# Performance work log

Measured on AMD Instinct MI355X. Metric: run time of the kernel, lower is better.

The kernel has to match this reference:

```python
import jax, jax.numpy as jnp
import numpy as np

B, T_IN, T_OUT = 32, 256, 512
N_MEL, E = 80, 512
A_RNN, D_RNN, PRENET, A_DIM = 1024, 1024, 256, 128
N_FILT, KSIZE = 32, 31


def setup_inputs() -> dict:
    key = jax.random.key(0)
    ks = jax.random.split(key, 20)
    def w(k, shape):
        fan_in = shape[-1] if len(shape) == 2 else shape[1] * shape[2]
        return jax.random.normal(k, shape, jnp.float32) / np.sqrt(fan_in)
    return dict(
        memory=jax.random.normal(ks[0], (B, T_IN, E), jnp.float32),
        decoder_inputs=jax.random.normal(ks[1], (B, N_MEL, T_OUT), jnp.float32),
        memory_lengths=jax.random.randint(ks[2], (B,), T_IN // 2, T_IN + 1).astype(jnp.int32),
        prenet_w1=w(ks[3], (PRENET, N_MEL)),
        prenet_w2=w(ks[4], (PRENET, PRENET)),
        att_rnn_wih=w(ks[5], (4 * A_RNN, PRENET + E)),
        att_rnn_whh=w(ks[6], (4 * A_RNN, A_RNN)),
        att_rnn_b=jnp.zeros((4 * A_RNN,), jnp.float32),
        wq=w(ks[7], (A_DIM, A_RNN)),
        wm=w(ks[8], (A_DIM, E)),
        v=w(ks[9], (1, A_DIM)),
        loc_conv=w(ks[10], (N_FILT, 2, KSIZE)),
        loc_dense=w(ks[11], (A_DIM, N_FILT)),
        dec_rnn_wih=w(ks[12], (4 * D_RNN, A_RNN + E)),
        dec_rnn_whh=w(ks[13], (4 * D_RNN, D_RNN)),
        dec_rnn_b=jnp.zeros((4 * D_RNN,), jnp.float32),
        proj_w=w(ks[14], (N_MEL, D_RNN + E)),
        proj_b=jnp.zeros((N_MEL,), jnp.float32),
        gate_w=w(ks[15], (1, D_RNN + E)),
        gate_b=jnp.zeros((1,), jnp.float32),
    )


def _lstm_cell(x, h, c, wih, whh, b):
    g = x @ wih.T + h @ whh.T + b
    i, f, gg, o = jnp.split(g, 4, axis=-1)
    c2 = jax.nn.sigmoid(f) * c + jax.nn.sigmoid(i) * jnp.tanh(gg)
    h2 = jax.nn.sigmoid(o) * jnp.tanh(c2)
    return h2, c2


def reference(memory, decoder_inputs, memory_lengths, prenet_w1, prenet_w2,
              att_rnn_wih, att_rnn_whh, att_rnn_b, wq, wm, v, loc_conv, loc_dense,
              dec_rnn_wih, dec_rnn_whh, dec_rnn_b, proj_w, proj_b, gate_w, gate_b):
    Bc, Tin, Ec = memory.shape
    # True where padded (masked out of attention)
    pad_mask = jnp.arange(Tin)[None, :] >= memory_lengths[:, None]
    processed_memory = memory @ wm.T  # (B, T_in, A_DIM)

    # parse decoder inputs: (B, n_mel, T_out) -> (T_out, B, n_mel); prepend go frame
    dec_seq = jnp.transpose(decoder_inputs, (2, 0, 1))
    go = jnp.zeros((1, Bc, N_MEL), dec_seq.dtype)
    dec_seq = jnp.concatenate([go, dec_seq], axis=0)[:-1]  # teacher-forced inputs
    # prenet (eval; stochastic dropout removed for determinism)
    x = jax.nn.relu(dec_seq @ prenet_w1.T)
    x = jax.nn.relu(x @ prenet_w2.T)  # (T_out, B, PRENET)

    NEG = jnp.asarray(-1e9, memory.dtype)
    pad = KSIZE // 2

    def step(carry, xt):
        ah, ac, dh, dc, aw, awc, ctx = carry
        # attention RNN
        ah, ac = _lstm_cell(jnp.concatenate([xt, ctx], -1), ah, ac,
                            att_rnn_wih, att_rnn_whh, att_rnn_b)
        # location-sensitive attention
        cat = jnp.stack([aw, awc], axis=1)  # (B, 2, T_in)
        loc = jax.lax.conv_general_dilated(cat, loc_conv, (1,), [(pad, pad)],
                                           dimension_numbers=('NCH', 'OIH', 'NCH'))
        loc = jnp.transpose(loc, (0, 2, 1)) @ loc_dense.T  # (B, T_in, A_DIM)
        pq = ah @ wq.T  # (B, A_DIM)
        e = jnp.tanh(pq[:, None, :] + loc + processed_memory) @ v[0]  # (B, T_in)
        e = jnp.where(pad_mask, NEG, e)
        wgt = jax.nn.softmax(e, axis=1)
        ctx = jnp.einsum('bt,bte->be', wgt, memory)
        awc = awc + wgt
        # decoder RNN
        dh, dc = _lstm_cell(jnp.concatenate([ah, ctx], -1), dh, dc,
                            dec_rnn_wih, dec_rnn_whh, dec_rnn_b)
        pi = jnp.concatenate([dh, ctx], -1)
        mel = pi @ proj_w.T + proj_b
        gate = (pi @ gate_w.T + gate_b)[:, 0]
        return (ah, ac, dh, dc, wgt, awc, ctx), (mel, gate, wgt)

    z = lambda *s: jnp.zeros(s, memory.dtype)
    carry0 = (z(Bc, A_RNN), z(Bc, A_RNN), z(Bc, D_RNN), z(Bc, D_RNN),
              z(Bc, Tin), z(Bc, Tin), z(Bc, Ec))
    _, (mels, gates, aligns) = jax.lax.scan(step, carry0, x)
    mel_out = jnp.transpose(mels, (1, 2, 0))      # (B, n_mel, T_out)
    gate_out = gates.T                             # (B, T_out)
    align_out = jnp.transpose(aligns, (1, 0, 2))   # (B, T_out, T_in)
    return mel_out, gate_out, align_out
```

## Files before the change

### kernel.cpp

```cpp
#include <hip/hip_runtime.h>
#include <hip/hip_bf16.h>
#include <math.h>

typedef __attribute__((ext_vector_type(8))) short bf16x8;
typedef __attribute__((ext_vector_type(4))) float f32x4;

#define B_X2    0u
#define B_PM    8388608u
#define B_WSA   12582912u
#define B_WSD   27262976u
#define B_AHB0  48234496u
#define B_AHB1  48300032u
#define B_DHB0  48365568u
#define B_DHB1  48431104u
#define B_CTXB  48496640u
#define B_AC    48529408u
#define B_DC    48660480u
#define B_AWC   48791552u
#define B_ZERO_START 48234496u
#define B_ZERO_BYTES 589824u
#define B_AHF   48824320u
#define B_DHF0  48955392u
#define B_CTXF0 49086464u
#define B_CTXF1 49152000u
#define B_DHF1  49217536u
#define B_LPM   49348608u
#define B_WQT   53542912u

#define OUT_MEL   0u
#define OUT_GATE  1310720u
#define OUT_ALIGN 1327104u

#define PSM_BYTES 6144

#define QSM_BYTES 23040

__device__ __forceinline__ float sigf(float x) { return 1.f / (1.f + expf(-x)); }
__device__ __forceinline__ float ftanh(float x) {
    float t = exp2f(x * 2.885390081777927f);
    return 1.f - 2.f * __builtin_amdgcn_rcpf(t + 1.f);
}

#define HOLD(s, b0, b1) (((s) & 1) ? (b0) : (b1))

__global__ __launch_bounds__(256) void prenet_kernel(
    const float* __restrict__ dec_in,
    const float* __restrict__ w1,
    const float* __restrict__ w2,
    __hip_bfloat16* __restrict__ x2)
{
    int b  = blockIdx.x & 31;
    int t0 = (blockIdx.x >> 5) * 16;
    __shared__ float xin[16][80];
    __shared__ float h1[16][257];

    for (int i = threadIdx.x; i < 16 * 80; i += 256) {
        int tt = i / 80, m = i - tt * 80;
        int t = t0 + tt;
        xin[tt][m] = (t == 0) ? 0.f
                   : dec_in[(size_t)b * 80 * 512 + (size_t)m * 512 + (t - 1)];
    }
    __syncthreads();
    for (int i = threadIdx.x; i < 16 * 256; i += 256) {
        int tt = i >> 8, p = i & 255;
        const float* wr = w1 + p * 80;
        float s = 0.f;
        for (int m = 0; m < 80; ++m) s += xin[tt][m] * wr[m];
        h1[tt][p] = fmaxf(s, 0.f);
    }
    __syncthreads();
    for (int i = threadIdx.x; i < 16 * 256; i += 256) {
        int tt = i >> 8, q = i & 255;
        const float* wr = w2 + q * 256;
        float s = 0.f;
        for (int p = 0; p < 256; ++p) s += h1[tt][p] * wr[p];
        int t = t0 + tt;
        x2[(size_t)t * (32 * 256) + b * 256 + q] = __float2bfloat16(fmaxf(s, 0.f));
    }
}

__global__ __launch_bounds__(128) void pm_kernel(
    const float* __restrict__ memory,
    const float* __restrict__ wm,
    float* __restrict__ pm)
{
    int b = blockIdx.y, tt0 = blockIdx.x * 16;
    __shared__ float ms[16][513];
    for (int i = threadIdx.x; i < 16 * 512; i += 128) {
        int tt = i >> 9, e = i & 511;
        ms[tt][e] = memory[(size_t)b * 131072 + (size_t)(tt0 + tt) * 512 + e];
    }
    __syncthreads();
    int d = threadIdx.x;
    float acc[16];
#pragma unroll
    for (int i = 0; i < 16; ++i) acc[i] = 0.f;
    const float* wr = wm + d * 512;
    for (int e = 0; e < 512; ++e) {
        float w = wr[e];
#pragma unroll
        for (int ttl = 0; ttl < 16; ++ttl) acc[ttl] += w * ms[ttl][e];
    }
    for (int ttl = 0; ttl < 16; ++ttl)
        pm[(size_t)b * 32768 + (size_t)(tt0 + ttl) * 128 + d] = acc[ttl];
}

__global__ __launch_bounds__(256) void swizzle_kernel(
    const float* __restrict__ wih, int Kih,
    const float* __restrict__ whh, int Khh,
    __hip_bfloat16* __restrict__ out, int K)
{
    int idx = blockIdx.x * 256 + threadIdx.x;
    int lane = idx & 63;
    int tk = idx >> 6;
    int KB = K >> 5;
    int nt = tk / KB, kb = tk - nt * KB;
    int c = lane & 15;
    int n = (c >> 2) * 1024 + nt * 4 + (c & 3);
    int k = kb * 32 + ((lane >> 4) << 3);
    const float* src; int kk;
    if (k < Kih) { src = wih + (size_t)n * Kih; kk = k; }
    else         { src = whh + (size_t)n * Khh; kk = k - Kih; }
    __hip_bfloat16* op = out + (size_t)idx * 8;
#pragma unroll
    for (int j = 0; j < 8; ++j) op[j] = __float2bfloat16(src[kk + j]);
}

__global__ __launch_bounds__(256) void wqt_kernel(
    const float* __restrict__ wq,
    float* __restrict__ wqT)
{
    int idx = blockIdx.x * 256 + threadIdx.x;
    int k = idx >> 7, d = idx & 127;
    wqT[idx] = wq[(size_t)d * 1024 + k];
}

template<int K, int S0, int S1, int S0STR, int S1STR, int S2STR>
__device__ __forceinline__ void lstm_tile(
    char* smem, int nt,
    const __hip_bfloat16* __restrict__ seg0,
    const __hip_bfloat16* __restrict__ seg1,
    const __hip_bfloat16* __restrict__ seg2,
    const __hip_bfloat16* __restrict__ wsw,
    const float* __restrict__ bias,
    float* __restrict__ c_state,
    float* __restrict__ h_f32,
    __hip_bfloat16* __restrict__ h_bf16)
{
    constexpr int KB  = K / 32;
    constexpr int NCH = K / 256;

    float (*red)[2][4][64] = (float(*)[2][4][64])smem;
    float (*gsum)[17]      = (float(*)[17])(smem + 16384);

    int tid  = threadIdx.x;
    int lane = tid & 63;
    int w    = tid >> 6;
    int r0   = lane & 15;
    int kq   = (lane >> 4) << 3;

    const __hip_bfloat16* wp = wsw + (((size_t)nt * KB + (size_t)w * NCH) * 64 + lane) * 8;
    f32x4 acc0 = {0.f, 0.f, 0.f, 0.f};
    f32x4 acc1 = {0.f, 0.f, 0.f, 0.f};
    int k0 = w * (K / 8);

#pragma unroll
    for (int i = 0; i < NCH; ++i) {
        int kc = k0 + i * 32;
        const __hip_bfloat16* sp; int sstr, off;
        if (kc < S0)           { sp = seg0; sstr = S0STR; off = kc; }
        else if (kc < S0 + S1) { sp = seg1; sstr = S1STR; off = kc - S0; }
        else                   { sp = seg2; sstr = S2STR; off = kc - S0 - S1; }
        int ko = off + kq;
        bf16x8 a0 = *(const bf16x8*)(sp + (size_t)r0 * sstr + ko);
        bf16x8 a1 = *(const bf16x8*)(sp + (size_t)(r0 + 16) * sstr + ko);
        bf16x8 bb = *(const bf16x8*)(wp + (size_t)i * 512);
        acc0 = __builtin_amdgcn_mfma_f32_16x16x32_bf16(a0, bb, acc0, 0, 0, 0);
        acc1 = __builtin_amdgcn_mfma_f32_16x16x32_bf16(a1, bb, acc1, 0, 0, 0);
    }

#pragma unroll
    for (int r = 0; r < 4; ++r) {
        red[w][0][r][lane] = acc0[r];
        red[w][1][r][lane] = acc1[r];
    }
    __syncthreads();

    {
        int b = tid >> 4, c = tid & 15;
        int mt = b >> 4, bm = b & 15;
        int lidx = ((bm >> 2) << 4) + c, rg = bm & 3;
        float s = 0.f;
#pragma unroll
        for (int ks = 0; ks < 8; ++ks) s += red[ks][mt][rg][lidx];
        gsum[b][c] = s;
    }
    __syncthreads();

    if (tid < 128) {
        int b = tid & 31, jl = tid >> 5;
        int j = nt * 4 + jl;
        float gi = gsum[b][jl]      + bias[j];
        float gf = gsum[b][4 + jl]  + bias[1024 + j];
        float gg = gsum[b][8 + jl]  + bias[2048 + j];
        float go = gsum[b][12 + jl] + bias[3072 + j];
        float cv = c_state[b * 1024 + j];
        float c2 = sigf(gf) * cv + sigf(gi) * tanhf(gg);
        float h2 = sigf(go) * tanhf(c2);
        c_state[b * 1024 + j] = c2;
        h_f32[b * 1024 + j]   = h2;
        h_bf16[b * 1024 + j]  = __float2bfloat16(h2);
    }
}

__global__ __launch_bounds__(1024) void pstep_kernel(
    const float* __restrict__ memory,
    const int*   __restrict__ mlen,
    const float* __restrict__ wqT,
    const float* __restrict__ v,
    const float* __restrict__ lpmbuf,
    const float* __restrict__ ahf,
    float* __restrict__ ctxf0, float* __restrict__ ctxf1,
    __hip_bfloat16* __restrict__ ctxb,
    float* __restrict__ awc,
    float* __restrict__ align_out,
    const float* __restrict__ dhf0, const float* __restrict__ dhf1,
    const float* __restrict__ proj_w, const float* __restrict__ proj_b,
    const float* __restrict__ gate_w, const float* __restrict__ gate_b,
    float* __restrict__ out_mel, float* __restrict__ out_gate,
    int t)
{
    __shared__ char smem[PSM_BYTES];
    int blk = blockIdx.x;
    int tid = threadIdx.x;

    if (blk < 32) {
        int b = blk;
        float* red   = (float*)smem;
        float* pq_s  = (float*)(smem + 4096);
        float* v_s   = (float*)(smem + 4608);
        float* wgt_s = (float*)(smem + 5120);

        int len = mlen[b];

        if (tid < 128) v_s[tid] = v[tid];
        {
            int p = tid >> 7, d = tid & 127;
            const float* wt = wqT + (size_t)(p * 128) * 128 + d;
            const float* hh = ahf + b * 1024 + p * 128;
            float s0 = 0.f, s1 = 0.f, s2 = 0.f, s3 = 0.f;
#pragma unroll 8
            for (int kk = 0; kk < 128; kk += 4) {
                s0 = fmaf(hh[kk],     wt[(size_t)kk * 128],       s0);
                s1 = fmaf(hh[kk + 1], wt[(size_t)(kk + 1) * 128], s1);
                s2 = fmaf(hh[kk + 2], wt[(size_t)(kk + 2) * 128], s2);
                s3 = fmaf(hh[kk + 3], wt[(size_t)(kk + 3) * 128], s3);
            }
            red[tid] = (s0 + s1) + (s2 + s3);
        }
        __syncthreads();

        if (tid < 128) {
            float s = 0.f;
#pragma unroll
            for (int p = 0; p < 8; ++p) s += red[p * 128 + tid];
            pq_s[tid] = s;
        }
        __syncthreads();

        {
            int ttc = tid >> 2, dg = tid & 3;
            const float4* lp4 = (const float4*)(lpmbuf + ((size_t)b << 15) + (size_t)ttc * 128 + dg * 32);
            const float4* pq4 = (const float4*)(pq_s + dg * 32);
            const float4* v4  = (const float4*)(v_s + dg * 32);
            float pe = 0.f;
#pragma unroll
            for (int j = 0; j < 8; ++j) {
                float4 x = lp4[j], pq = pq4[j], vv = v4[j];
                pe += ftanh(x.x + pq.x) * vv.x + ftanh(x.y + pq.y) * vv.y
                    + ftanh(x.z + pq.z) * vv.z + ftanh(x.w + pq.w) * vv.w;
            }
            __syncthreads();
            red[tid] = pe;
        }
        __syncthreads();

        if (tid < 64) {
            float ev[4];
            float mx = -1e30f;
#pragma unroll
            for (int r = 0; r < 4; ++r) {
                int tt = tid * 4 + r;
                float e = red[tt * 4] + red[tt * 4 + 1] + red[tt * 4 + 2] + red[tt * 4 + 3];
                ev[r] = (tt < len) ? e : -1e9f;
                mx = fmaxf(mx, ev[r]);
            }
#pragma unroll
            for (int mm = 32; mm >= 1; mm >>= 1) mx = fmaxf(mx, __shfl_xor(mx, mm));
            float sum = 0.f;
#pragma unroll
            for (int r = 0; r < 4; ++r) {
                ev[r] = exp2f((ev[r] - mx) * 1.4426950408889634f);
                sum += ev[r];
            }
#pragma unroll
            for (int mm = 32; mm >= 1; mm >>= 1) sum += __shfl_xor(sum, mm);
            float winv = __builtin_amdgcn_rcpf(sum);
#pragma unroll
            for (int r = 0; r < 4; ++r) {
                int tt = tid * 4 + r;
                float wg = ev[r] * winv;
                wgt_s[tt] = wg;
                align_out[(size_t)b * 131072 + (size_t)t * 256 + tt] = wg;
                awc[b * 256 + tt] += wg;
            }
        }
        __syncthreads();

        {
            int ee = tid & 511, p = tid >> 9;
            const float* mr = memory + (size_t)b * 131072 + ee;
            float s0 = 0.f, s1 = 0.f, s2 = 0.f, s3 = 0.f;
            float s4 = 0.f, s5 = 0.f, s6 = 0.f, s7 = 0.f;
            int t0 = p * 128;
            for (int ttl = 0; ttl < 128; ttl += 8) {
                int tt = t0 + ttl;
                s0 = fmaf(wgt_s[tt],     mr[(size_t)tt * 512],       s0);
                s1 = fmaf(wgt_s[tt + 1], mr[(size_t)(tt + 1) * 512], s1);
                s2 = fmaf(wgt_s[tt + 2], mr[(size_t)(tt + 2) * 512], s2);
                s3 = fmaf(wgt_s[tt + 3], mr[(size_t)(tt + 3) * 512], s3);
                s4 = fmaf(wgt_s[tt + 4], mr[(size_t)(tt + 4) * 512], s4);
                s5 = fmaf(wgt_s[tt + 5], mr[(size_t)(tt + 5) * 512], s5);
                s6 = fmaf(wgt_s[tt + 6], mr[(size_t)(tt + 6) * 512], s6);
                s7 = fmaf(wgt_s[tt + 7], mr[(size_t)(tt + 7) * 512], s7);
            }
            red[p * 512 + ee] = ((s0 + s1) + (s2 + s3)) + ((s4 + s5) + (s6 + s7));
        }
        __syncthreads();
        if (tid < 512) {
            float cv = red[tid] + red[512 + tid];
            float* ctxf_cur = HOLD(t, ctxf1, ctxf0);
            ctxf_cur[b * 512 + tid] = cv;
            ctxb[b * 512 + tid] = __float2bfloat16(cv);
        }
        return;
    }

    {
        if (t < 1) return;
        int pb = blk - 32;
        int b = pb >> 1, half = pb & 1;
        int tp = t - 1;
        const float* dh = HOLD(tp, dhf1, dhf0);
        const float* cx = HOLD(tp, ctxf1, ctxf0);
        float* pi = (float*)smem;
        if (tid < 1024) pi[tid] = dh[b * 1024 + tid];
        else ;
        if (tid < 512) pi[1024 + tid] = cx[b * 512 + tid];
        __syncthreads();
        int w = tid >> 6, lane = tid & 63;
        int nOut = half ? 41 : 40;
        for (int o = w; o < nOut; o += 16) {
            bool isGate = (half && o == 40);
            int m = half * 40 + o;
            const float* wr = isGate ? gate_w : (proj_w + (size_t)m * 1536);
            float s = 0.f;
#pragma unroll
            for (int c = 0; c < 6; ++c) {
                float4 wv = *(const float4*)(wr + c * 256 + lane * 4);
                const float* pp = pi + c * 256 + lane * 4;
                s += wv.x * pp[0] + wv.y * pp[1] + wv.z * pp[2] + wv.w * pp[3];
            }
#pragma unroll
            for (int mm = 32; mm >= 1; mm >>= 1) s += __shfl_xor(s, mm);
            if (lane == 0) {
                if (isGate) out_gate[b * 512 + tp] = s + gate_b[0];
                else out_mel[(size_t)b * (80 * 512) + (size_t)m * 512 + tp]
                        = s + proj_b[m];
            }
        }
    }
}

__global__ __launch_bounds__(512, 2) void qstep_kernel(
    const __hip_bfloat16* __restrict__ x2b,
    __hip_bfloat16* __restrict__ ctxb,
    __hip_bfloat16* __restrict__ ahb0, __hip_bfloat16* __restrict__ ahb1,
    __hip_bfloat16* __restrict__ dhb0, __hip_bfloat16* __restrict__ dhb1,
    const __hip_bfloat16* __restrict__ wswA,
    const __hip_bfloat16* __restrict__ wswD,
    const float* __restrict__ a_b, const float* __restrict__ d_b,
    float* __restrict__ ac, float* __restrict__ dc,
    float* __restrict__ ahf,
    float* __restrict__ dhf0, float* __restrict__ dhf1,
    const float* __restrict__ lconv, const float* __restrict__ ldense,
    const float* __restrict__ pm,
    const float* __restrict__ awc, const float* __restrict__ align_out,
    float* __restrict__ lpmbuf,
    int t)
{
    __shared__ char smem[QSM_BYTES];
    int blk = blockIdx.x;
    int tid = threadIdx.x;

    if (blk < 256) {
        if (t < 0) return;
        lstm_tile<2560, 1024, 512, 1024, 512, 1024>(
            smem, blk,
            HOLD(t, ahb0, ahb1), ctxb, HOLD(t - 1, dhb0, dhb1),
            wswD, d_b, dc,
            HOLD(t, dhf1, dhf0), HOLD(t, dhb0, dhb1));
        return;
    }

    if (blk < 384) {
        int s = t + 1;
        if (s > 511) return;
        int base = (blk - 256) * 2;
#pragma unroll
        for (int h = 0; h < 2; ++h) {
            if (h) __syncthreads();
            lstm_tile<1792, 256, 512, 256, 512, 1024>(
                smem, base + h,
                x2b + (size_t)s * 8192, ctxb, HOLD(s - 1, ahb0, ahb1),
                wswA, a_b, ac, ahf, HOLD(s, ahb0, ahb1));
        }
        return;
    }

    {
        if (t + 1 > 511) return;
        int b = blk - 384;
        __hip_bfloat16 (*locb)[40] = (__hip_bfloat16(*)[40])smem;
        float* aw_s  = (float*)(smem + 20480);
        float* awc_s = (float*)(smem + 21632);

        if (tid < 288) {
            int tt = tid - 15;
            float a = 0.f, c = 0.f;
            if (tt >= 0 && tt < 256) {
                a = (t >= 0) ? align_out[(size_t)b * 131072 + (size_t)t * 256 + tt] : 0.f;
                c = awc[b * 256 + tt];
            }
            aw_s[tid] = a; awc_s[tid] = c;
        }
        __syncthreads();

        for (int it = 0; it < 2; ++it) {
            int item = tid + it * 512;
            int f = item >> 5, ttg = item & 31;
            const float* kcA = lconv + f * 62;
            const float* kcB = kcA + 31;
            float ka[31], kb_[31];
#pragma unroll
            for (int k = 0; k < 31; ++k) { ka[k] = kcA[k]; kb_[k] = kcB[k]; }
            float acc[8];
#pragma unroll
            for (int s = 0; s < 8; ++s) acc[s] = 0.f;
            int base = ttg * 8;
#pragma unroll
            for (int u = 0; u < 38; ++u) {
                float av = aw_s[base + u];
                float cv = awc_s[base + u];
#pragma unroll
                for (int s = 0; s < 8; ++s) {
                    int k = u - s;
                    if (k >= 0 && k < 31) {
                        acc[s] = fmaf(ka[k], av, acc[s]);
                        acc[s] = fmaf(kb_[k], cv, acc[s]);
                    }
                }
            }
#pragma unroll
            for (int s = 0; s < 8; ++s)
                locb[base + s][f] = __float2bfloat16(acc[s]);
        }
        __syncthreads();

        {
            int lane = tid & 63;
            int w    = tid >> 6;
            int c    = lane & 15, q = lane >> 4;

            bf16x8 Bf[8];
#pragma unroll
            for (int tc = 0; tc < 8; ++tc) {
                int d = tc * 16 + c;
                const float* lp = ldense + d * 32 + q * 8;
                float4 f0 = *(const float4*)lp;
                float4 f1 = *(const float4*)(lp + 4);
                union { bf16x8 vv; __hip_bfloat16 h[8]; } u;
                u.h[0] = __float2bfloat16(f0.x); u.h[1] = __float2bfloat16(f0.y);
                u.h[2] = __float2bfloat16(f0.z); u.h[3] = __float2bfloat16(f0.w);
                u.h[4] = __float2bfloat16(f1.x); u.h[5] = __float2bfloat16(f1.y);
                u.h[6] = __float2bfloat16(f1.z); u.h[7] = __float2bfloat16(f1.w);
                Bf[tc] = u.vv;
            }
#pragma unroll
            for (int half = 0; half < 2; ++half) {
                int mt = w * 2 + half;
                bf16x8 Af = *(const bf16x8*)&locb[mt * 16 + c][q * 8];
                f32x4 zero = {0.f, 0.f, 0.f, 0.f};
#pragma unroll
                for (int tc = 0; tc < 8; ++tc) {
                    f32x4 P = __builtin_amdgcn_mfma_f32_16x16x32_bf16(Af, Bf[tc], zero, 0, 0, 0);
                    int d = tc * 16 + c;
#pragma unroll
                    for (int r = 0; r < 4; ++r) {
                        int ttp = mt * 16 + q * 4 + r;
                        size_t ix = ((size_t)b << 15) + (size_t)ttp * 128 + d;
                        lpmbuf[ix] = P[r] + pm[ix];
                    }
                }
            }
        }
    }
}

__global__ __launch_bounds__(256) void proj_kernel(
    const float* __restrict__ dh,
    const float* __restrict__ ctx,
    const float* __restrict__ proj_w,
    const float* __restrict__ proj_b,
    const float* __restrict__ gate_w,
    const float* __restrict__ gate_b,
    float* __restrict__ out_mel,
    float* __restrict__ out_gate,
    int t)
{
    int b = blockIdx.x, tid = threadIdx.x;
    __shared__ float pi[1536];
    __shared__ float red[256];
    for (int i = tid; i < 1024; i += 256) pi[i] = dh[b * 1024 + i];
    for (int i = tid; i < 512; i += 256) pi[1024 + i] = ctx[b * 512 + i];
    __syncthreads();

    float s = 0.f;
    if (tid < 240) {
        int m = tid / 3, p = tid - m * 3;
        const float* wr = proj_w + (size_t)m * 1536 + p * 512;
        const float* pr = pi + p * 512;
        for (int k = 0; k < 512; ++k) s += wr[k] * pr[k];
    } else {
        int p = tid - 240;
        const float* wr = gate_w + p * 96;
        const float* pr = pi + p * 96;
        for (int k = 0; k < 96; ++k) s += wr[k] * pr[k];
    }
    red[tid] = s;
    __syncthreads();
    if (tid < 80) {
        float m3 = red[tid * 3] + red[tid * 3 + 1] + red[tid * 3 + 2];
        out_mel[(size_t)b * (80 * 512) + (size_t)tid * 512 + t] = m3 + proj_b[tid];
    } else if (tid == 80) {
        float g = gate_b[0];
#pragma unroll
        for (int p = 0; p < 16; ++p) g += red[240 + p];
        out_gate[b * 512 + t] = g;
    }
}

extern "C" void kernel_launch(void* const* d_in, const int* in_sizes, int n_in,
                              void* d_out, int out_size, void* d_ws, size_t ws_size,
                              hipStream_t stream)
{
    const float* memory   = (const float*)d_in[0];
    const float* dec_in   = (const float*)d_in[1];
    const int*   mlen     = (const int*)  d_in[2];
    const float* pw1      = (const float*)d_in[3];
    const float* pw2      = (const float*)d_in[4];
    const float* a_wih    = (const float*)d_in[5];
    const float* a_whh    = (const float*)d_in[6];
    const float* a_b      = (const float*)d_in[7];
    const float* wq       = (const float*)d_in[8];
    const float* wm       = (const float*)d_in[9];
    const float* v        = (const float*)d_in[10];
    const float* lconv    = (const float*)d_in[11];
    const float* ldense   = (const float*)d_in[12];
    const float* d_wih    = (const float*)d_in[13];
    const float* d_whh    = (const float*)d_in[14];
    const float* d_b      = (const float*)d_in[15];
    const float* proj_w   = (const float*)d_in[16];
    const float* proj_b   = (const float*)d_in[17];
    const float* gate_w   = (const float*)d_in[18];
    const float* gate_b   = (const float*)d_in[19];

    char* ws = (char*)d_ws;
    __hip_bfloat16* x2b  = (__hip_bfloat16*)(ws + B_X2);
    float*          pm   = (float*)(ws + B_PM);
    __hip_bfloat16* wswA = (__hip_bfloat16*)(ws + B_WSA);
    __hip_bfloat16* wswD = (__hip_bfloat16*)(ws + B_WSD);
    __hip_bfloat16* ahb0 = (__hip_bfloat16*)(ws + B_AHB0);
    __hip_bfloat16* ahb1 = (__hip_bfloat16*)(ws + B_AHB1);
    __hip_bfloat16* dhb0 = (__hip_bfloat16*)(ws + B_DHB0);
    __hip_bfloat16* dhb1 = (__hip_bfloat16*)(ws + B_DHB1);
    __hip_bfloat16* ctxb = (__hip_bfloat16*)(ws + B_CTXB);
    float*          ac   = (float*)(ws + B_AC);
    float*          dc   = (float*)(ws + B_DC);
    float*          awcp = (float*)(ws + B_AWC);
    float*          ahf  = (float*)(ws + B_AHF);
    float*          dhf0 = (float*)(ws + B_DHF0);
    float*          dhf1 = (float*)(ws + B_DHF1);
    float*          ctxf0= (float*)(ws + B_CTXF0);
    float*          ctxf1= (float*)(ws + B_CTXF1);
    float*          lpmb = (float*)(ws + B_LPM);
    float*          wqt  = (float*)(ws + B_WQT);

    float* out       = (float*)d_out;
    float* out_mel   = out + OUT_MEL;
    float* out_gate  = out + OUT_GATE;
    float* out_align = out + OUT_ALIGN;

    hipMemsetAsync(ws + B_ZERO_START, 0, B_ZERO_BYTES, stream);

    prenet_kernel<<<1024, 256, 0, stream>>>(dec_in, pw1, pw2, x2b);
    pm_kernel<<<dim3(16, 32), 128, 0, stream>>>(memory, wm, pm);
    swizzle_kernel<<<3584, 256, 0, stream>>>(a_wih, 768,  a_whh, 1024, wswA, 1792);
    swizzle_kernel<<<5120, 256, 0, stream>>>(d_wih, 1536, d_whh, 1024, wswD, 2560);
    wqt_kernel<<<512, 256, 0, stream>>>(wq, wqt);

    qstep_kernel<<<416, 512, 0, stream>>>(
        x2b, ctxb, ahb0, ahb1, dhb0, dhb1, wswA, wswD, a_b, d_b,
        ac, dc, ahf, dhf0, dhf1,
        lconv, ldense, pm, awcp, out_align, lpmb, -1);

    for (int t = 0; t < 512; ++t) {
        pstep_kernel<<<96, 1024, 0, stream>>>(
            memory, mlen, wqt, v, lpmb, ahf,
            ctxf0, ctxf1, ctxb, awcp, out_align,
            dhf0, dhf1,
            proj_w, proj_b, gate_w, gate_b, out_mel, out_gate, t);

        qstep_kernel<<<416, 512, 0, stream>>>(
            x2b, ctxb, ahb0, ahb1, dhb0, dhb1, wswA, wswD, a_b, d_b,
            ac, dc, ahf, dhf0, dhf1,
            lconv, ldense, pm, awcp, out_align, lpmb, t);
    }

    proj_kernel<<<32, 256, 0, stream>>>(
        dhf1, ctxf1, proj_w, proj_b, gate_w, gate_b,
        out_mel, out_gate, 511);
}
```

Measured before the change: 22.76 ms.

## Fuse location conv and dense into attention step kernel, spread LSTM tiles wider

Moves the location-sensitive convolution and its MFMA dense projection from the qstep kernel into the pstep attention blocks. The upper 512 threads run it right after the softmax, while the lower 512 threads compute the context vector over all 256 timesteps without a shared reduction. The attention-weight inputs now come from shared memory instead of being re-read from align_out. The qstep kernel is relaunched with 512 blocks so each attention-LSTM tile gets its own block rather than two per block, and the initial location buffer is seeded with a device copy of processed memory. The intent is to shorten the serial per-step chain and raise LSTM parallelism, at the cost of more work and shared memory in each pstep attention block.

Measured after the change: 24.63 ms. +8.2%, slower.

```diff
diff --git a/kernel.cpp b/kernel.cpp
--- a/kernel.cpp
+++ b/kernel.cpp
@@ -31,9 +31,9 @@
 #define OUT_GATE  1310720u
 #define OUT_ALIGN 1327104u
 
-#define PSM_BYTES 6144
-
-#define QSM_BYTES 23040
+#define PSM_BYTES 27776
+
+#define QSM_BYTES 18560
 
 __device__ __forceinline__ float sigf(float x) { return 1.f / (1.f + expf(-x)); }
 __device__ __forceinline__ float ftanh(float x) {
@@ -218,12 +218,14 @@
     const int*   __restrict__ mlen,
     const float* __restrict__ wqT,
     const float* __restrict__ v,
-    const float* __restrict__ lpmbuf,
+    float* __restrict__ lpmbuf,
     const float* __restrict__ ahf,
     float* __restrict__ ctxf0, float* __restrict__ ctxf1,
     __hip_bfloat16* __restrict__ ctxb,
     float* __restrict__ awc,
     float* __restrict__ align_out,
+    const float* __restrict__ lconv, const float* __restrict__ ldense,
+    const float* __restrict__ pm,
     const float* __restrict__ dhf0, const float* __restrict__ dhf1,
     const float* __restrict__ proj_w, const float* __restrict__ proj_b,
     const float* __restrict__ gate_w, const float* __restrict__ gate_b,
@@ -236,14 +238,20 @@
 
     if (blk < 32) {
         int b = blk;
-        float* red   = (float*)smem;
-        float* pq_s  = (float*)(smem + 4096);
-        float* v_s   = (float*)(smem + 4608);
-        float* wgt_s = (float*)(smem + 5120);
+        __hip_bfloat16 (*locb)[40] = (__hip_bfloat16(*)[40])smem;
+        float* red   = (float*)(smem + 20480);
+        float* pq_s  = (float*)(smem + 24576);
+        float* v_s   = (float*)(smem + 25088);
+        float* wgt_s = (float*)(smem + 25600);
+        float* awc_s = (float*)(smem + 26624);
 
         int len = mlen[b];
 
         if (tid < 128) v_s[tid] = v[tid];
+        if (tid < 288) {
+            int tt = tid - 15;
+            awc_s[tid] = (tt >= 0 && tt < 256) ? awc[b * 256 + tt] : 0.f;
+        }
         {
             int p = tid >> 7, d = tid & 127;
             const float* wt = wqT + (size_t)(p * 128) * 128 + d;
@@ -317,14 +325,12 @@
         }
         __syncthreads();
 
-        {
-            int ee = tid & 511, p = tid >> 9;
-            const float* mr = memory + (size_t)b * 131072 + ee;
+        if (tid < 512) {
+            int e = tid;
+            const float* mr = memory + (size_t)b * 131072 + e;
             float s0 = 0.f, s1 = 0.f, s2 = 0.f, s3 = 0.f;
             float s4 = 0.f, s5 = 0.f, s6 = 0.f, s7 = 0.f;
-            int t0 = p * 128;
-            for (int ttl = 0; ttl < 128; ttl += 8) {
-                int tt = t0 + ttl;
+            for (int tt = 0; tt < 256; tt += 8) {
                 s0 = fmaf(wgt_s[tt],     mr[(size_t)tt * 512],       s0);
                 s1 = fmaf(wgt_s[tt + 1], mr[(size_t)(tt + 1) * 512], s1);
                 s2 = fmaf(wgt_s[tt + 2], mr[(size_t)(tt + 2) * 512], s2);
@@ -334,14 +340,82 @@
                 s6 = fmaf(wgt_s[tt + 6], mr[(size_t)(tt + 6) * 512], s6);
                 s7 = fmaf(wgt_s[tt + 7], mr[(size_t)(tt + 7) * 512], s7);
             }
-            red[p * 512 + ee] = ((s0 + s1) + (s2 + s3)) + ((s4 + s5) + (s6 + s7));
-        }
-        __syncthreads();
-        if (tid < 512) {
-            float cv = red[tid] + red[512 + tid];
+            float cv = ((s0 + s1) + (s2 + s3)) + ((s4 + s5) + (s6 + s7));
             float* ctxf_cur = HOLD(t, ctxf1, ctxf0);
-            ctxf_cur[b * 512 + tid] = cv;
-            ctxb[b * 512 + tid] = __float2bfloat16(cv);
+            ctxf_cur[b * 512 + e] = cv;
+            ctxb[b * 512 + e] = __float2bfloat16(cv);
+        } else if (t < 511) {
+            int tid2 = tid - 512;
+            int w8   = tid2 >> 6;
+            int lane = tid2 & 63;
+
+#pragma unroll
+            for (int half = 0; half < 2; ++half) {
+                int j = half * 64 + lane;
+                int ttg = 4 * w8 + (j >> 5);
+                int f = j & 31;
+                const float* kcA = lconv + f * 62;
+                const float* kcB = kcA + 31;
+                float ka[31], kb_[31];
+#pragma unroll
+                for (int k = 0; k < 31; ++k) { ka[k] = kcA[k]; kb_[k] = kcB[k]; }
+                float acc[8];
+#pragma unroll
+                for (int s = 0; s < 8; ++s) acc[s] = 0.f;
+                int base = ttg * 8;
+#pragma unroll
+                for (int u = 0; u < 38; ++u) {
+                    int ttx = base + u - 15;
+                    float av = (ttx >= 0 && ttx < 256) ? wgt_s[ttx] : 0.f;
+                    float cvv = awc_s[base + u] + av;
+#pragma unroll
+                    for (int s = 0; s < 8; ++s) {
+                        int k = u - s;
+                        if (k >= 0 && k < 31) {
+                            acc[s] = fmaf(ka[k], av, acc[s]);
+                            acc[s] = fmaf(kb_[k], cvv, acc[s]);
+                        }
+                    }
+                }
+#pragma unroll
+                for (int s = 0; s < 8; ++s)
+                    locb[base + s][f] = __float2bfloat16(acc[s]);
+            }
+
+            {
+                int c = lane & 15, q = lane >> 4;
+                bf16x8 Bf[8];
+#pragma unroll
+                for (int tc = 0; tc < 8; ++tc) {
+                    int d = tc * 16 + c;
+                    const float* lp = ldense + d * 32 + q * 8;
+                    float4 f0 = *(const float4*)lp;
+                    float4 f1 = *(const float4*)(lp + 4);
+                    union { bf16x8 vv; __hip_bfloat16 h[8]; } u;
+                    u.h[0] = __float2bfloat16(f0.x); u.h[1] = __float2bfloat16(f0.y);
+                    u.h[2] = __float2bfloat16(f0.z); u.h[3] = __float2bfloat16(f0.w);
+                    u.h[4] = __float2bfloat16(f1.x); u.h[5] = __float2bfloat16(f1.y);
+                    u.h[6] = __float2bfloat16(f1.z); u.h[7] = __float2bfloat16(f1.w);
+                    Bf[tc] = u.vv;
+                }
+#pragma unroll
+                for (int halfm = 0; halfm < 2; ++halfm) {
+                    int mt = 2 * w8 + halfm;
+                    bf16x8 Af = *(const bf16x8*)&locb[mt * 16 + c][q * 8];
+                    f32x4 zero = {0.f, 0.f, 0.f, 0.f};
+#pragma unroll
+                    for (int tc = 0; tc < 8; ++tc) {
+                        f32x4 P = __builtin_amdgcn_mfma_f32_16x16x32_bf16(Af, Bf[tc], zero, 0, 0, 0);
+                        int d = tc * 16 + c;
+#pragma unroll
+                        for (int r = 0; r < 4; ++r) {
+                            int ttp = mt * 16 + q * 4 + r;
+                            size_t ix = ((size_t)b << 15) + (size_t)ttp * 128 + d;
+                            lpmbuf[ix] = P[r] + pm[ix];
+                        }
+                    }
+                }
+            }
         }
         return;
     }
@@ -355,7 +429,6 @@
         const float* cx = HOLD(tp, ctxf1, ctxf0);
         float* pi = (float*)smem;
         if (tid < 1024) pi[tid] = dh[b * 1024 + tid];
-        else ;
         if (tid < 512) pi[1024 + tid] = cx[b * 512 + tid];
         __syncthreads();
         int w = tid >> 6, lane = tid & 63;
@@ -393,15 +466,10 @@
     float* __restrict__ ac, float* __restrict__ dc,
     float* __restrict__ ahf,
     float* __restrict__ dhf0, float* __restrict__ dhf1,
-    const float* __restrict__ lconv, const float* __restrict__ ldense,
-    const float* __restrict__ pm,
-    const float* __restrict__ awc, const float* __restrict__ align_out,
-    float* __restrict__ lpmbuf,
     int t)
 {
     __shared__ char smem[QSM_BYTES];
     int blk = blockIdx.x;
-    int tid = threadIdx.x;
 
     if (blk < 256) {
         if (t < 0) return;
@@ -413,107 +481,13 @@
         return;
     }
 
-    if (blk < 384) {
+    {
         int s = t + 1;
         if (s > 511) return;
-        int base = (blk - 256) * 2;
-#pragma unroll
-        for (int h = 0; h < 2; ++h) {
-            if (h) __syncthreads();
-            lstm_tile<1792, 256, 512, 256, 512, 1024>(
-                smem, base + h,
-                x2b + (size_t)s * 8192, ctxb, HOLD(s - 1, ahb0, ahb1),
-                wswA, a_b, ac, ahf, HOLD(s, ahb0, ahb1));
-        }
-        return;
-    }
-
-    {
-        if (t + 1 > 511) return;
-        int b = blk - 384;
-        __hip_bfloat16 (*locb)[40] = (__hip_bfloat16(*)[40])smem;
-        float* aw_s  = (float*)(smem + 20480);
-        float* awc_s = (float*)(smem + 21632);
-
-        if (tid < 288) {
-            int tt = tid - 15;
-            float a = 0.f, c = 0.f;
-            if (tt >= 0 && tt < 256) {
-                a = (t >= 0) ? align_out[(size_t)b * 131072 + (size_t)t * 256 + tt] : 0.f;
-                c = awc[b * 256 + tt];
-            }
-            aw_s[tid] = a; awc_s[tid] = c;
-        }
-        __syncthreads();
-
-        for (int it = 0; it < 2; ++it) {
-            int item = tid + it * 512;
-            int f = item >> 5, ttg = item & 31;
-            const float* kcA = lconv + f * 62;
-            const float* kcB = kcA + 31;
-            float ka[31], kb_[31];
-#pragma unroll
-            for (int k = 0; k < 31; ++k) { ka[k] = kcA[k]; kb_[k] = kcB[k]; }
-            float acc[8];
-#pragma unroll
-            for (int s = 0; s < 8; ++s) acc[s] = 0.f;
-            int base = ttg * 8;
-#pragma unroll
-            for (int u = 0; u < 38; ++u) {
-                float av = aw_s[base + u];
-                float cv = awc_s[base + u];
-#pragma unroll
-                for (int s = 0; s < 8; ++s) {
-                    int k = u - s;
-                    if (k >= 0 && k < 31) {
-                        acc[s] = fmaf(ka[k], av, acc[s]);
-                        acc[s] = fmaf(kb_[k], cv, acc[s]);
-                    }
-                }
-            }
-#pragma unroll
-            for (int s = 0; s < 8; ++s)
-                locb[base + s][f] = __float2bfloat16(acc[s]);
-        }
-        __syncthreads();
-
-        {
-            int lane = tid & 63;
-            int w    = tid >> 6;
-            int c    = lane & 15, q = lane >> 4;
-
-            bf16x8 Bf[8];
-#pragma unroll
-            for (int tc = 0; tc < 8; ++tc) {
-                int d = tc * 16 + c;
-                const float* lp = ldense + d * 32 + q * 8;
-                float4 f0 = *(const float4*)lp;
-                float4 f1 = *(const float4*)(lp + 4);
-                union { bf16x8 vv; __hip_bfloat16 h[8]; } u;
-                u.h[0] = __float2bfloat16(f0.x); u.h[1] = __float2bfloat16(f0.y);
-                u.h[2] = __float2bfloat16(f0.z); u.h[3] = __float2bfloat16(f0.w);
-                u.h[4] = __float2bfloat16(f1.x); u.h[5] = __float2bfloat16(f1.y);
-                u.h[6] = __float2bfloat16(f1.z); u.h[7] = __float2bfloat16(f1.w);
-                Bf[tc] = u.vv;
-            }
-#pragma unroll
-            for (int half = 0; half < 2; ++half) {
-                int mt = w * 2 + half;
-                bf16x8 Af = *(const bf16x8*)&locb[mt * 16 + c][q * 8];
-                f32x4 zero = {0.f, 0.f, 0.f, 0.f};
-#pragma unroll
-                for (int tc = 0; tc < 8; ++tc) {
-                    f32x4 P = __builtin_amdgcn_mfma_f32_16x16x32_bf16(Af, Bf[tc], zero, 0, 0, 0);
-                    int d = tc * 16 + c;
-#pragma unroll
-                    for (int r = 0; r < 4; ++r) {
-                        int ttp = mt * 16 + q * 4 + r;
-                        size_t ix = ((size_t)b << 15) + (size_t)ttp * 128 + d;
-                        lpmbuf[ix] = P[r] + pm[ix];
-                    }
-                }
-            }
-        }
+        lstm_tile<1792, 256, 512, 256, 512, 1024>(
+            smem, blk - 256,
+            x2b + (size_t)s * 8192, ctxb, HOLD(s - 1, ahb0, ahb1),
+            wswA, a_b, ac, ahf, HOLD(s, ahb0, ahb1));
     }
 }
 
@@ -619,22 +593,22 @@
     swizzle_kernel<<<5120, 256, 0, stream>>>(d_wih, 1536, d_whh, 1024, wswD, 2560);
     wqt_kernel<<<512, 256, 0, stream>>>(wq, wqt);
 
-    qstep_kernel<<<416, 512, 0, stream>>>(
+    hipMemcpyAsync(lpmb, pm, 4194304, hipMemcpyDeviceToDevice, stream);
+    qstep_kernel<<<512, 512, 0, stream>>>(
         x2b, ctxb, ahb0, ahb1, dhb0, dhb1, wswA, wswD, a_b, d_b,
-        ac, dc, ahf, dhf0, dhf1,
-        lconv, ldense, pm, awcp, out_align, lpmb, -1);
+        ac, dc, ahf, dhf0, dhf1, -1);
 
     for (int t = 0; t < 512; ++t) {
         pstep_kernel<<<96, 1024, 0, stream>>>(
             memory, mlen, wqt, v, lpmb, ahf,
             ctxf0, ctxf1, ctxb, awcp, out_align,
+            lconv, ldense, pm,
             dhf0, dhf1,
             proj_w, proj_b, gate_w, gate_b, out_mel, out_gate, t);
 
-        qstep_kernel<<<416, 512, 0, stream>>>(
+        qstep_kernel<<<512, 512, 0, stream>>>(
             x2b, ctxb, ahb0, ahb1, dhb0, dhb1, wswA, wswD, a_b, d_b,
-            ac, dc, ahf, dhf0, dhf1,
-            lconv, ldense, pm, awcp, out_align, lpmb, t);
+            ac, dc, ahf, dhf0, dhf1, t);
     }
 
     proj_kernel<<<32, 256, 0, stream>>>(
```
